# Kernel tuning notes

Hardware: AMD Instinct MI355X
Metric: run time of the kernel (lower is better)

Reference implementation:

```python
import jax, jax.numpy as jnp
import numpy as np

N, F, FE, NB = 50000, 64, 64, 16
E, T = 1_600_000, 1_000_000
IN_DIM = F + 2 * FE + NB  # 208
VAR = 0.15
EPS = 1e-5  # BatchNorm eps


def setup_inputs() -> dict:
    key = jax.random.key(0)
    ks = jax.random.split(key, 10)
    atom_fea = jax.random.normal(ks[0], (N, F), dtype=jnp.float32)
    edge_fea = jax.random.normal(ks[1], (E, FE), dtype=jnp.float32)
    r_ij = jax.random.normal(ks[2], (E, 3), dtype=jnp.float32)
    dist = jax.random.uniform(ks[3], (E,), dtype=jnp.float32, minval=0.5, maxval=5.0)
    cutoff_w = jax.random.uniform(ks[4], (E,), dtype=jnp.float32)
    fc_w = jax.random.normal(ks[5], (2 * F, IN_DIM), dtype=jnp.float32) / np.sqrt(IN_DIM)
    fc_b = jax.random.normal(ks[6], (2 * F,), dtype=jnp.float32) * 0.01
    bn1_gamma = jnp.ones((2 * F,), jnp.float32)
    bn1_beta = jnp.zeros((2 * F,), jnp.float32)
    bn2_gamma = jnp.ones((F,), jnp.float32)
    bn2_beta = jnp.zeros((F,), jnp.float32)
    edge_index = jax.random.randint(ks[7], (2, E), 0, N, dtype=jnp.int32)
    triplet_idx = jax.random.randint(ks[8], (2, T), 0, E, dtype=jnp.int32)
    return dict(atom_fea=atom_fea, edge_fea=edge_fea, r_ij=r_ij, dist=dist,
                cutoff_w=cutoff_w, fc_w=fc_w, fc_b=fc_b,
                bn1_gamma=bn1_gamma, bn1_beta=bn1_beta,
                bn2_gamma=bn2_gamma, bn2_beta=bn2_beta,
                edge_index=edge_index, triplet_idx=triplet_idx)


def _batchnorm(x, gamma, beta):
    # training-mode BatchNorm1d: biased batch statistics
    mu = x.mean(axis=0)
    var = ((x - mu) ** 2).mean(axis=0)
    return (x - mu) * jax.lax.rsqrt(var + EPS) * gamma + beta


def reference(atom_fea, edge_fea, r_ij, dist, cutoff_w, fc_w, fc_b,
              bn1_gamma, bn1_beta, bn2_gamma, bn2_beta,
              edge_index, triplet_idx):
    e1, e2 = triplet_idx[0], triplet_idx[1]
    dst = edge_index[1]
    # angle between neighbour displacement vectors
    v1 = r_ij[e1]            # (T,3)
    v2 = r_ij[e2]            # (T,3)
    d1 = jnp.maximum(dist[e1], 1e-8)
    d2 = jnp.maximum(dist[e2], 1e-8)
    cos_angle = jnp.clip((v1 * v2).sum(-1) / (d1 * d2), -1.0, 1.0)  # (T,)
    centers = jnp.linspace(-1.0, 1.0, NB)
    ang_fea = jnp.exp(-((cos_angle[:, None] - centers) ** 2) / (VAR ** 2))  # (T,NB)
    centre_atoms = dst[e1]   # (T,)
    triplet_fea = jnp.concatenate(
        [atom_fea[centre_atoms], edge_fea[e1], edge_fea[e2], ang_fea], axis=1)  # (T, IN_DIM)
    triplet_fea = _batchnorm(triplet_fea @ fc_w.T + fc_b, bn1_gamma, bn1_beta)  # (T, 2F)
    gate = jax.nn.sigmoid(triplet_fea[:, :F])
    core = jax.nn.softplus(triplet_fea[:, F:])
    messages = gate * core
    messages = messages * (cutoff_w[e1] * cutoff_w[e2])[:, None]
    aggr = jax.ops.segment_sum(messages, centre_atoms, num_segments=N)  # (N,F)
    aggr = _batchnorm(aggr, bn2_gamma, bn2_beta)
    return jax.nn.softplus(atom_fea + aggr)
```

## Files before the change

kernel.cpp:

```cpp
#include <hip/hip_runtime.h>
#include <hip/hip_bf16.h>
#include <math.h>

typedef __bf16 bf16;
typedef __bf16 bf16x8 __attribute__((ext_vector_type(8)));
typedef float  f32x4  __attribute__((ext_vector_type(4)));
typedef float  f32x4e __attribute__((ext_vector_type(4)));

#define MT     64
#define ROWPAD 232
#define NREP   32

union PK8 { bf16 h[8]; uint4 u; };
union PKH { _Float16 h[2]; unsigned int u; };

__device__ inline uint4 pack8(const float4 a, const float4 b) {
  PK8 p;
  p.h[0] = (bf16)a.x; p.h[1] = (bf16)a.y; p.h[2] = (bf16)a.z; p.h[3] = (bf16)a.w;
  p.h[4] = (bf16)b.x; p.h[5] = (bf16)b.y; p.h[6] = (bf16)b.z; p.h[7] = (bf16)b.w;
  return p.u;
}

__device__ inline bf16x8 zero_bf16x8() {
  PK8 z; z.u = make_uint4(0u, 0u, 0u, 0u);
  return *(bf16x8*)z.h;
}

__global__ __launch_bounds__(256)
void k_cvt(const float* __restrict__ src, bf16* __restrict__ dst, long n8) {
  const long i = (long)blockIdx.x * 256 + threadIdx.x;
  if (i >= n8) return;
  const f32x4e a = __builtin_nontemporal_load((const f32x4e*)(src + i * 8));
  const f32x4e b = __builtin_nontemporal_load((const f32x4e*)(src + i * 8 + 4));
  PK8 p;
#pragma unroll
  for (int j = 0; j < 4; ++j) { p.h[j] = (bf16)a[j]; p.h[4 + j] = (bf16)b[j]; }
  *(uint4*)(dst + i * 8) = p.u;
}

__global__ __launch_bounds__(256)
void k_cvtw(const float* __restrict__ fc_w, bf16* __restrict__ dst) {
  const int i = blockIdx.x * 256 + threadIdx.x;
  if (i >= 128 * 28) return;
  const int row = i / 28, c = i - row * 28;
  uint4 v;
  if (c < 26) {
    const float4* p = (const float4*)(fc_w + (size_t)row * 208 + c * 8);
    v = pack8(p[0], p[1]);
  } else {
    v = make_uint4(0u, 0u, 0u, 0u);
  }
  *(uint4*)(dst + (size_t)row * 224 + c * 8) = v;
}

template<bool PRE>
__global__ __launch_bounds__(256)
void k_gemm(const float* __restrict__ atom_fea,
            const float* __restrict__ edge_fea,
            const bf16*  __restrict__ atom_bf,
            const bf16*  __restrict__ edge_bf,
            const float* __restrict__ r_ij,
            const float* __restrict__ dist,
            const float* __restrict__ cutoff_w,
            const float* __restrict__ fc_w,
            const bf16*  __restrict__ fcw_bf,
            const float* __restrict__ fc_b,
            const int*  __restrict__ eidx_dst,
            const int*  __restrict__ trip_e1,
            const int*  __restrict__ trip_e2,
            float* __restrict__ stat1,
            unsigned int* __restrict__ zbuf,
            int*   __restrict__ centre,
            float* __restrict__ cwbuf)
{
  __shared__ __align__(16) bf16 smA[MT * ROWPAD];

  const int tid  = threadIdx.x;
  const int lane = tid & 63;
  const int wv   = tid >> 6;
  const int quad = lane >> 4;
  const int l16  = lane & 15;
  const int t0   = blockIdx.x * MT;

  bf16x8 bfrag[2][7];
  float  bias_v[2];
#pragma unroll
  for (int ns = 0; ns < 2; ++ns) {
    const int col = wv * 32 + ns * 16 + l16;
    bias_v[ns] = fc_b[col];
#pragma unroll
    for (int kc = 0; kc < 7; ++kc) {
      if (PRE) {
        bfrag[ns][kc] = *(const bf16x8*)(fcw_bf + (size_t)col * 224 + kc * 32 + quad * 8);
      } else {
        const int k0 = kc * 32 + quad * 8;
        if (k0 < 208) {
          const float4* p = (const float4*)(fc_w + (size_t)col * 208 + k0);
          PK8 pk; pk.u = pack8(p[0], p[1]);
          bfrag[ns][kc] = *(bf16x8*)pk.h;
        } else {
          bfrag[ns][kc] = zero_bf16x8();
        }
      }
    }
  }

  if (PRE) {
    const int row = tid >> 2;
    const int cq  = tid & 3;
    const int t   = t0 + row;
    const int e1  = trip_e1[t];
    const int e2  = trip_e2[t];
    const int ca  = eidx_dst[e1];
    const bf16* ar = atom_bf + (size_t)ca * 64;
    const bf16* r1 = edge_bf + (size_t)e1 * 64;
    const bf16* r2 = edge_bf + (size_t)e2 * 64;
    const uint4 v0 = *(const uint4*)(ar + cq * 8);
    const uint4 v1 = *(const uint4*)(ar + (cq + 4) * 8);
    const uint4 v2 = *(const uint4*)(r1 + cq * 8);
    const uint4 v3 = *(const uint4*)(r1 + (cq + 4) * 8);
    const uint4 v4 = *(const uint4*)(r2 + cq * 8);
    const uint4 v5 = *(const uint4*)(r2 + (cq + 4) * 8);
    bf16* dstr = smA + row * ROWPAD;
    if (cq == 0) {
      const float x1 = r_ij[e1 * 3], y1 = r_ij[e1 * 3 + 1], z1 = r_ij[e1 * 3 + 2];
      const float x2 = r_ij[e2 * 3], y2 = r_ij[e2 * 3 + 1], z2 = r_ij[e2 * 3 + 2];
      const float d1 = fmaxf(dist[e1], 1e-8f);
      const float d2 = fmaxf(dist[e2], 1e-8f);
      float cv = (x1 * x2 + y1 * y2 + z1 * z2) / (d1 * d2);
      cv = fminf(1.f, fmaxf(-1.f, cv));
      PK8 pa, pb;
#pragma unroll
      for (int j = 0; j < 8; ++j) {
        const float ca0 = cv - (-1.f + (float)j * (2.f / 15.f));
        const float ca1 = cv - (-1.f + (float)(j + 8) * (2.f / 15.f));
        pa.h[j] = (bf16)__expf(-(ca0 * ca0) * 44.4444444f);
        pb.h[j] = (bf16)__expf(-(ca1 * ca1) * 44.4444444f);
      }
      *(uint4*)(dstr + 24 * 8) = pa.u;
      *(uint4*)(dstr + 25 * 8) = pb.u;
      centre[t] = ca;
      cwbuf[t] = cutoff_w[e1] * cutoff_w[e2];
    } else if (cq == 2) {
      *(uint4*)(dstr + 26 * 8) = make_uint4(0u, 0u, 0u, 0u);
    } else if (cq == 3) {
      *(uint4*)(dstr + 27 * 8) = make_uint4(0u, 0u, 0u, 0u);
    }
    *(uint4*)(dstr + cq * 8)        = v0;
    *(uint4*)(dstr + (cq + 4) * 8)  = v1;
    *(uint4*)(dstr + (cq + 8) * 8)  = v2;
    *(uint4*)(dstr + (cq + 12) * 8) = v3;
    *(uint4*)(dstr + (cq + 16) * 8) = v4;
    *(uint4*)(dstr + (cq + 20) * 8) = v5;
  } else {
    for (int i = tid; i < MT * 28; i += 256) {
      const int row = i / 28;
      const int c   = i - row * 28;
      const int t   = t0 + row;
      uint4 val;
      if (c < 8) {
        const int e1 = trip_e1[t];
        const int ca = eidx_dst[e1];
        const float4* p = (const float4*)(atom_fea + (size_t)ca * 64 + c * 8);
        val = pack8(p[0], p[1]);
        if (c == 0) {
          const int e2 = trip_e2[t];
          centre[t] = ca;
          cwbuf[t] = cutoff_w[e1] * cutoff_w[e2];
        }
      } else if (c < 16) {
        const int e1 = trip_e1[t];
        const float4* p = (const float4*)(edge_fea + (size_t)e1 * 64 + (c - 8) * 8);
        val = pack8(p[0], p[1]);
      } else if (c < 24) {
        const int e2 = trip_e2[t];
        const float4* p = (const float4*)(edge_fea + (size_t)e2 * 64 + (c - 16) * 8);
        val = pack8(p[0], p[1]);
      } else if (c < 26) {
        const int e1 = trip_e1[t];
        const int e2 = trip_e2[t];
        const float x1 = r_ij[e1 * 3], y1 = r_ij[e1 * 3 + 1], z1 = r_ij[e1 * 3 + 2];
        const float x2 = r_ij[e2 * 3], y2 = r_ij[e2 * 3 + 1], z2 = r_ij[e2 * 3 + 2];
        const float d1 = fmaxf(dist[e1], 1e-8f);
        const float d2 = fmaxf(dist[e2], 1e-8f);
        float cv = (x1 * x2 + y1 * y2 + z1 * z2) / (d1 * d2);
        cv = fminf(1.f, fmaxf(-1.f, cv));
        PK8 p;
        const int b0 = (c - 24) * 8;
#pragma unroll
        for (int j = 0; j < 8; ++j) {
          const float ctr = -1.f + (float)(b0 + j) * (2.f / 15.f);
          const float dd = cv - ctr;
          p.h[j] = (bf16)__expf(-(dd * dd) * 44.4444444f);
        }
        val = p.u;
      } else {
        val = make_uint4(0u, 0u, 0u, 0u);
      }
      *(uint4*)(smA + row * ROWPAD + c * 8) = val;
    }
  }
  __syncthreads();

  f32x4 acc[4][2] = {};
#pragma unroll
  for (int kc = 0; kc < 7; ++kc) {
    bf16x8 afr[4];
#pragma unroll
    for (int ms = 0; ms < 4; ++ms)
      afr[ms] = *(const bf16x8*)(smA + (ms * 16 + l16) * ROWPAD + kc * 32 + quad * 8);
#pragma unroll
    for (int ms = 0; ms < 4; ++ms)
#pragma unroll
      for (int ns = 0; ns < 2; ++ns)
        acc[ms][ns] = __builtin_amdgcn_mfma_f32_16x16x32_bf16(afr[ms], bfrag[ns][kc], acc[ms][ns], 0, 0, 0);
  }

  unsigned int* zw = zbuf + (size_t)t0 * 64;
  float s0 = 0.f, s20 = 0.f, s1 = 0.f, s21 = 0.f;
#pragma unroll
  for (int ms = 0; ms < 4; ++ms)
#pragma unroll
    for (int r = 0; r < 4; ++r) {
      const float z0 = acc[ms][0][r] + bias_v[0];
      const float z1 = acc[ms][1][r] + bias_v[1];
      PKH pk; pk.h[0] = (_Float16)z0; pk.h[1] = (_Float16)z1;
      const int row = ms * 16 + quad * 4 + r;
      __builtin_nontemporal_store(pk.u, zw + (size_t)row * 64 + wv * 16 + l16);
      s0 += z0; s20 += z0 * z0; s1 += z1; s21 += z1 * z1;
    }
  s0  += __shfl_xor(s0, 16);  s0  += __shfl_xor(s0, 32);
  s20 += __shfl_xor(s20, 16); s20 += __shfl_xor(s20, 32);
  s1  += __shfl_xor(s1, 16);  s1  += __shfl_xor(s1, 32);
  s21 += __shfl_xor(s21, 16); s21 += __shfl_xor(s21, 32);
  if (quad == 0) {
    float* sb = stat1 + (size_t)(blockIdx.x & (NREP - 1)) * 256;
    const int c0 = wv * 32 + l16;
    atomicAdd(sb + c0, s0);
    atomicAdd(sb + 128 + c0, s20);
    atomicAdd(sb + c0 + 16, s1);
    atomicAdd(sb + 128 + c0 + 16, s21);
  }
}

__global__ void k_fin1(const float* __restrict__ stat1,
                       const float* __restrict__ g1, const float* __restrict__ b1,
                       float* __restrict__ bn1sc, float* __restrict__ bn1sh, float invT) {
  const int j = threadIdx.x;
  float s = 0.f, s2 = 0.f;
  for (int r = 0; r < NREP; ++r) { s += stat1[r * 256 + j]; s2 += stat1[r * 256 + 128 + j]; }
  const float mu  = s * invT;
  const float var = fmaxf(s2 * invT - mu * mu, 0.f);
  const float sc  = g1[j] * rsqrtf(var + 1e-5f);
  bn1sc[j] = sc;
  bn1sh[j] = b1[j] - mu * sc;
}

__global__ __launch_bounds__(256)
void k_apply(const unsigned int* __restrict__ zbuf,
             const int*   __restrict__ centre,
             const float* __restrict__ cwbuf,
             const float* __restrict__ bn1sc, const float* __restrict__ bn1sh,
             float* __restrict__ aggr, size_t repN, int T)
{
  const int lane = threadIdx.x & 63;
  const int sub  = threadIdx.x >> 6;
  const int f    = lane;
  const int wg   = ((f >> 5) << 4) | (f & 15);
  const int sel  = (f >> 4) & 1;
  const float scg = bn1sc[f],      shg = bn1sh[f];
  const float scc = bn1sc[64 + f], shc = bn1sh[64 + f];
  float* ag = aggr + (size_t)(blockIdx.x & 1) * repN;
  for (int t = blockIdx.x * 4 + sub; t < T; t += gridDim.x * 4) {
    const unsigned int ug = __builtin_nontemporal_load(zbuf + (size_t)t * 64 + wg);
    const unsigned int uc = __builtin_nontemporal_load(zbuf + (size_t)t * 64 + 32 + wg);
    PKH a, b; a.u = ug; b.u = uc;
    const float zg = (sel ? (float)a.h[1] : (float)a.h[0]) * scg + shg;
    const float zc = (sel ? (float)b.h[1] : (float)b.h[0]) * scc + shc;
    const float gate = 1.f / (1.f + __expf(-zg));
    const float core = (zc > 20.f) ? zc : log1pf(__expf(zc));
    atomicAdd(ag + (size_t)centre[t] * 64 + f, gate * core * cwbuf[t]);
  }
}

__global__ __launch_bounds__(256)
void k_bn2stats(float* __restrict__ aggr, size_t repN, float* __restrict__ stat2, int N) {
  const int col = threadIdx.x & 63;
  const int rg  = threadIdx.x >> 6;
  float s = 0.f, s2 = 0.f;
  for (int n = blockIdx.x * 4 + rg; n < N; n += gridDim.x * 4) {
    const size_t idx = (size_t)n * 64 + col;
    const float v = aggr[idx] + aggr[repN + idx];
    aggr[idx] = v;
    s += v; s2 += v * v;
  }
  __shared__ float ps[4][64], ps2[4][64];
  ps[rg][col] = s; ps2[rg][col] = s2;
  __syncthreads();
  if (rg == 0) {
    s  = ps[0][col] + ps[1][col] + ps[2][col] + ps[3][col];
    s2 = ps2[0][col] + ps2[1][col] + ps2[2][col] + ps2[3][col];
    atomicAdd(stat2 + col, s);
    atomicAdd(stat2 + 64 + col, s2);
  }
}

__global__ __launch_bounds__(256)
void k_final(const float* __restrict__ aggr, const float* __restrict__ atom,
             const float* __restrict__ stat2,
             const float* __restrict__ g2, const float* __restrict__ b2,
             float* __restrict__ out, int total, float invN) {
  const int idx = blockIdx.x * 256 + threadIdx.x;
  if (idx >= total) return;
  const int col = idx & 63;
  const float mu  = stat2[col] * invN;
  const float var = fmaxf(stat2[64 + col] * invN - mu * mu, 0.f);
  const float sc  = g2[col] * rsqrtf(var + 1e-5f);
  const float sh  = b2[col] - mu * sc;
  const float x   = aggr[idx] * sc + sh + atom[idx];
  out[idx] = (x > 20.f) ? x : log1pf(__expf(x));
}

extern "C" void kernel_launch(void* const* d_in, const int* in_sizes, int n_in,
                              void* d_out, int out_size, void* d_ws, size_t ws_size,
                              hipStream_t stream) {
  const float* atom_fea = (const float*)d_in[0];
  const float* edge_fea = (const float*)d_in[1];
  const float* r_ij     = (const float*)d_in[2];
  const float* dist     = (const float*)d_in[3];
  const float* cutoff_w = (const float*)d_in[4];
  const float* fc_w     = (const float*)d_in[5];
  const float* fc_b     = (const float*)d_in[6];
  const float* bn1g     = (const float*)d_in[7];
  const float* bn1b     = (const float*)d_in[8];
  const float* bn2g     = (const float*)d_in[9];
  const float* bn2b     = (const float*)d_in[10];
  const int*  eidx      = (const int*)d_in[11];
  const int*  tidx      = (const int*)d_in[12];

  const int N = in_sizes[0] / 64;
  const int E = in_sizes[3];
  const int T = in_sizes[12] / 2;

  const size_t repN = (size_t)N * 64;

  size_t off = 0;
  char* base = (char*)d_ws;
  auto carve = [&](size_t bytes) -> void* {
    void* p = base + off;
    off += (bytes + 255) & ~(size_t)255;
    return p;
  };
  float* aggr    = (float*)carve(2 * repN * 4);
  float* stat1   = (float*)carve((size_t)NREP * 256 * 4);
  float* bn1sc   = (float*)carve(128 * 4);
  float* bn1sh   = (float*)carve(128 * 4);
  float* stat2   = (float*)carve(128 * 4);
  float* cwbuf   = (float*)carve((size_t)T * 4);
  int*   centre  = (int*)carve((size_t)T * 4);
  unsigned int* zbuf = (unsigned int*)carve((size_t)T * 64 * 4);
  bf16*  edge_bf = (bf16*)carve((size_t)E * 64 * 2);
  bf16*  atom_bf = (bf16*)carve((size_t)N * 64 * 2);
  bf16*  fcw_bf  = (bf16*)carve((size_t)128 * 224 * 2);
  const bool pre = (off <= ws_size);

  hipMemsetAsync(aggr,  0, 2 * repN * sizeof(float), stream);
  hipMemsetAsync(stat1, 0, (size_t)NREP * 256 * sizeof(float), stream);
  hipMemsetAsync(stat2, 0, 128 * sizeof(float), stream);

  const int nblk = T / MT;
  if (pre) {
    const long e8 = (long)E * 64 / 8;
    const long a8 = (long)N * 64 / 8;
    k_cvt<<<(int)((e8 + 255) / 256), 256, 0, stream>>>(edge_fea, edge_bf, e8);
    k_cvt<<<(int)((a8 + 255) / 256), 256, 0, stream>>>(atom_fea, atom_bf, a8);
    k_cvtw<<<14, 256, 0, stream>>>(fc_w, fcw_bf);
    k_gemm<true><<<nblk, 256, 0, stream>>>(atom_fea, edge_fea, atom_bf, edge_bf,
                                           r_ij, dist, cutoff_w, fc_w, fcw_bf, fc_b,
                                           eidx + E, tidx, tidx + T,
                                           stat1, zbuf, centre, cwbuf);
  } else {
    k_gemm<false><<<nblk, 256, 0, stream>>>(atom_fea, edge_fea, atom_bf, edge_bf,
                                            r_ij, dist, cutoff_w, fc_w, fcw_bf, fc_b,
                                            eidx + E, tidx, tidx + T,
                                            stat1, zbuf, centre, cwbuf);
  }
  k_fin1<<<1, 128, 0, stream>>>(stat1, bn1g, bn1b, bn1sc, bn1sh, 1.0f / (float)T);
  k_apply<<<4096, 256, 0, stream>>>(zbuf, centre, cwbuf, bn1sc, bn1sh, aggr, repN, T);
  k_bn2stats<<<256, 256, 0, stream>>>(aggr, repN, stat2, N);
  const int total = N * 64;
  k_final<<<(total + 255) / 256, 256, 0, stream>>>(aggr, atom_fea, stat2, bn2g, bn2b,
                                                   (float*)d_out, total, 1.0f / (float)N);
}
```

Measured before the change: 1.099 ms.

## Replace atomic segment-sum with counting-sort CSR segmented reduction

```diff
diff --git a/kernel.cpp b/kernel.cpp
--- a/kernel.cpp
+++ b/kernel.cpp
@@ -24,6 +24,13 @@
 __device__ inline bf16x8 zero_bf16x8() {
   PK8 z; z.u = make_uint4(0u, 0u, 0u, 0u);
   return *(bf16x8*)z.h;
+}
+
+__device__ inline float fsigmoid(float x) {
+  return __builtin_amdgcn_rcpf(1.f + __expf(-x));
+}
+__device__ inline float fsoftplus(float x) {
+  return (x > 20.f) ? x : __logf(1.f + __expf(x));
 }
 
 __global__ __launch_bounds__(256)
@@ -53,6 +60,67 @@
   *(uint4*)(dst + (size_t)row * 224 + c * 8) = v;
 }
 
+__global__ __launch_bounds__(256)
+void k_prep(const int* __restrict__ trip_e1, const int* __restrict__ trip_e2,
+            const int* __restrict__ eidx_dst, const float* __restrict__ cutoff_w,
+            int* __restrict__ centre, float* __restrict__ cwbuf,
+            int* __restrict__ cnt, int T) {
+  for (int t = blockIdx.x * 256 + threadIdx.x; t < T; t += gridDim.x * 256) {
+    const int e1 = trip_e1[t];
+    const int e2 = trip_e2[t];
+    const int ca = eidx_dst[e1];
+    centre[t] = ca;
+    cwbuf[t] = cutoff_w[e1] * cutoff_w[e2];
+    atomicAdd(cnt + ca, 1);
+  }
+}
+
+__global__ __launch_bounds__(1024)
+void k_scan(const int* __restrict__ cnt, int* __restrict__ off,
+            int* __restrict__ cnt2, int N) {
+  __shared__ int part[1024];
+  const int tid = threadIdx.x;
+  const int CH  = (N + 1023) >> 10;
+  const int base = tid * CH;
+  int s = 0;
+  for (int i = 0; i < CH; ++i) {
+    const int idx = base + i;
+    if (idx < N) s += cnt[idx];
+  }
+  part[tid] = s;
+  __syncthreads();
+  for (int d = 1; d < 1024; d <<= 1) {
+    const int v = part[tid];
+    const int w = (tid >= d) ? part[tid - d] : 0;
+    __syncthreads();
+    part[tid] = v + w;
+    __syncthreads();
+  }
+  int run = (tid == 0) ? 0 : part[tid - 1];
+  for (int i = 0; i < CH; ++i) {
+    const int idx = base + i;
+    if (idx < N) {
+      const int c = cnt[idx];
+      off[idx] = run;
+      cnt2[idx] = run;
+      run += c;
+    }
+  }
+  if (tid == 1023) off[N] = run;
+}
+
+__global__ __launch_bounds__(256)
+void k_scatter(const int* __restrict__ centre, const float* __restrict__ cwbuf,
+               int* __restrict__ cnt2, int* __restrict__ post,
+               float* __restrict__ cw_s, int T) {
+  for (int t = blockIdx.x * 256 + threadIdx.x; t < T; t += gridDim.x * 256) {
+    const int c = centre[t];
+    const int p = atomicAdd(cnt2 + c, 1);
+    post[t] = p;
+    cw_s[p] = cwbuf[t];
+  }
+}
+
 template<bool PRE>
 __global__ __launch_bounds__(256)
 void k_gemm(const float* __restrict__ atom_fea,
@@ -61,19 +129,18 @@
             const bf16*  __restrict__ edge_bf,
             const float* __restrict__ r_ij,
             const float* __restrict__ dist,
-            const float* __restrict__ cutoff_w,
             const float* __restrict__ fc_w,
             const bf16*  __restrict__ fcw_bf,
             const float* __restrict__ fc_b,
-            const int*  __restrict__ eidx_dst,
             const int*  __restrict__ trip_e1,
             const int*  __restrict__ trip_e2,
+            const int*  __restrict__ centre,
+            const int*  __restrict__ post,
             float* __restrict__ stat1,
-            unsigned int* __restrict__ zbuf,
-            int*   __restrict__ centre,
-            float* __restrict__ cwbuf)
+            unsigned int* __restrict__ zbuf)
 {
   __shared__ __align__(16) bf16 smA[MT * ROWPAD];
+  __shared__ int sPos[MT];
 
   const int tid  = threadIdx.x;
   const int lane = tid & 63;
@@ -111,7 +178,7 @@
     const int t   = t0 + row;
     const int e1  = trip_e1[t];
     const int e2  = trip_e2[t];
-    const int ca  = eidx_dst[e1];
+    const int ca  = centre[t];
     const bf16* ar = atom_bf + (size_t)ca * 64;
     const bf16* r1 = edge_bf + (size_t)e1 * 64;
     const bf16* r2 = edge_bf + (size_t)e2 * 64;
@@ -139,8 +206,7 @@
       }
       *(uint4*)(dstr + 24 * 8) = pa.u;
       *(uint4*)(dstr + 25 * 8) = pb.u;
-      centre[t] = ca;
-      cwbuf[t] = cutoff_w[e1] * cutoff_w[e2];
+      sPos[row] = post[t];
     } else if (cq == 2) {
       *(uint4*)(dstr + 26 * 8) = make_uint4(0u, 0u, 0u, 0u);
     } else if (cq == 3) {
@@ -159,15 +225,10 @@
       const int t   = t0 + row;
       uint4 val;
       if (c < 8) {
-        const int e1 = trip_e1[t];
-        const int ca = eidx_dst[e1];
+        const int ca = centre[t];
         const float4* p = (const float4*)(atom_fea + (size_t)ca * 64 + c * 8);
         val = pack8(p[0], p[1]);
-        if (c == 0) {
-          const int e2 = trip_e2[t];
-          centre[t] = ca;
-          cwbuf[t] = cutoff_w[e1] * cutoff_w[e2];
-        }
+        if (c == 0) sPos[row] = post[t];
       } else if (c < 16) {
         const int e1 = trip_e1[t];
         const float4* p = (const float4*)(edge_fea + (size_t)e1 * 64 + (c - 8) * 8);
@@ -216,7 +277,6 @@
         acc[ms][ns] = __builtin_amdgcn_mfma_f32_16x16x32_bf16(afr[ms], bfrag[ns][kc], acc[ms][ns], 0, 0, 0);
   }
 
-  unsigned int* zw = zbuf + (size_t)t0 * 64;
   float s0 = 0.f, s20 = 0.f, s1 = 0.f, s21 = 0.f;
 #pragma unroll
   for (int ms = 0; ms < 4; ++ms)
@@ -226,7 +286,7 @@
       const float z1 = acc[ms][1][r] + bias_v[1];
       PKH pk; pk.h[0] = (_Float16)z0; pk.h[1] = (_Float16)z1;
       const int row = ms * 16 + quad * 4 + r;
-      __builtin_nontemporal_store(pk.u, zw + (size_t)row * 64 + wv * 16 + l16);
+      __builtin_nontemporal_store(pk.u, zbuf + (size_t)sPos[row] * 64 + wv * 16 + l16);
       s0 += z0; s20 += z0 * z0; s1 += z1; s21 += z1 * z1;
     }
   s0  += __shfl_xor(s0, 16);  s0  += __shfl_xor(s0, 32);
@@ -257,41 +317,39 @@
 }
 
 __global__ __launch_bounds__(256)
-void k_apply(const unsigned int* __restrict__ zbuf,
-             const int*   __restrict__ centre,
-             const float* __restrict__ cwbuf,
-             const float* __restrict__ bn1sc, const float* __restrict__ bn1sh,
-             float* __restrict__ aggr, size_t repN, int T)
+void k_apply2(const unsigned int* __restrict__ zbuf,
+              const int*   __restrict__ off,
+              const float* __restrict__ cw_s,
+              const float* __restrict__ bn1sc, const float* __restrict__ bn1sh,
+              float* __restrict__ aggr, int N)
 {
-  const int lane = threadIdx.x & 63;
-  const int sub  = threadIdx.x >> 6;
-  const int f    = lane;
-  const int wg   = ((f >> 5) << 4) | (f & 15);
-  const int sel  = (f >> 4) & 1;
+  const int n = (blockIdx.x << 2) | (threadIdx.x >> 6);
+  if (n >= N) return;
+  const int f   = threadIdx.x & 63;
+  const int wg  = ((f >> 5) << 4) | (f & 15);
+  const int sel = (f >> 4) & 1;
   const float scg = bn1sc[f],      shg = bn1sh[f];
   const float scc = bn1sc[64 + f], shc = bn1sh[64 + f];
-  float* ag = aggr + (size_t)(blockIdx.x & 1) * repN;
-  for (int t = blockIdx.x * 4 + sub; t < T; t += gridDim.x * 4) {
-    const unsigned int ug = __builtin_nontemporal_load(zbuf + (size_t)t * 64 + wg);
-    const unsigned int uc = __builtin_nontemporal_load(zbuf + (size_t)t * 64 + 32 + wg);
+  const int i0 = off[n], i1 = off[n + 1];
+  float acc = 0.f;
+  for (int i = i0; i < i1; ++i) {
+    const unsigned int ug = __builtin_nontemporal_load(zbuf + (size_t)i * 64 + wg);
+    const unsigned int uc = __builtin_nontemporal_load(zbuf + (size_t)i * 64 + 32 + wg);
     PKH a, b; a.u = ug; b.u = uc;
     const float zg = (sel ? (float)a.h[1] : (float)a.h[0]) * scg + shg;
     const float zc = (sel ? (float)b.h[1] : (float)b.h[0]) * scc + shc;
-    const float gate = 1.f / (1.f + __expf(-zg));
-    const float core = (zc > 20.f) ? zc : log1pf(__expf(zc));
-    atomicAdd(ag + (size_t)centre[t] * 64 + f, gate * core * cwbuf[t]);
-  }
-}
-
-__global__ __launch_bounds__(256)
-void k_bn2stats(float* __restrict__ aggr, size_t repN, float* __restrict__ stat2, int N) {
+    acc += fsigmoid(zg) * fsoftplus(zc) * cw_s[i];
+  }
+  aggr[(size_t)n * 64 + f] = acc;
+}
+
+__global__ __launch_bounds__(256)
+void k_bn2stats(const float* __restrict__ aggr, float* __restrict__ stat2, int N) {
   const int col = threadIdx.x & 63;
   const int rg  = threadIdx.x >> 6;
   float s = 0.f, s2 = 0.f;
   for (int n = blockIdx.x * 4 + rg; n < N; n += gridDim.x * 4) {
-    const size_t idx = (size_t)n * 64 + col;
-    const float v = aggr[idx] + aggr[repN + idx];
-    aggr[idx] = v;
+    const float v = aggr[(size_t)n * 64 + col];
     s += v; s2 += v * v;
   }
   __shared__ float ps[4][64], ps2[4][64];
@@ -318,7 +376,7 @@
   const float sc  = g2[col] * rsqrtf(var + 1e-5f);
   const float sh  = b2[col] - mu * sc;
   const float x   = aggr[idx] * sc + sh + atom[idx];
-  out[idx] = (x > 20.f) ? x : log1pf(__expf(x));
+  out[idx] = fsoftplus(x);
 }
 
 extern "C" void kernel_launch(void* const* d_in, const int* in_sizes, int n_in,
@@ -342,29 +400,32 @@
   const int E = in_sizes[3];
   const int T = in_sizes[12] / 2;
 
-  const size_t repN = (size_t)N * 64;
-
-  size_t off = 0;
+  size_t off_b = 0;
   char* base = (char*)d_ws;
   auto carve = [&](size_t bytes) -> void* {
-    void* p = base + off;
-    off += (bytes + 255) & ~(size_t)255;
+    void* p = base + off_b;
+    off_b += (bytes + 255) & ~(size_t)255;
     return p;
   };
-  float* aggr    = (float*)carve(2 * repN * 4);
+  float* aggr    = (float*)carve((size_t)N * 64 * 4);
   float* stat1   = (float*)carve((size_t)NREP * 256 * 4);
   float* bn1sc   = (float*)carve(128 * 4);
   float* bn1sh   = (float*)carve(128 * 4);
   float* stat2   = (float*)carve(128 * 4);
+  int*   cnt     = (int*)carve((size_t)N * 4);
+  int*   offs    = (int*)carve((size_t)(N + 1) * 4);
+  int*   cnt2    = (int*)carve((size_t)N * 4);
+  int*   centre  = (int*)carve((size_t)T * 4);
   float* cwbuf   = (float*)carve((size_t)T * 4);
-  int*   centre  = (int*)carve((size_t)T * 4);
+  int*   post    = (int*)carve((size_t)T * 4);
+  float* cw_s    = (float*)carve((size_t)T * 4);
   unsigned int* zbuf = (unsigned int*)carve((size_t)T * 64 * 4);
   bf16*  edge_bf = (bf16*)carve((size_t)E * 64 * 2);
   bf16*  atom_bf = (bf16*)carve((size_t)N * 64 * 2);
   bf16*  fcw_bf  = (bf16*)carve((size_t)128 * 224 * 2);
-  const bool pre = (off <= ws_size);
-
-  hipMemsetAsync(aggr,  0, 2 * repN * sizeof(float), stream);
+  const bool pre = (off_b <= ws_size);
+
+  hipMemsetAsync(cnt,   0, (size_t)N * 4, stream);
   hipMemsetAsync(stat1, 0, (size_t)NREP * 256 * sizeof(float), stream);
   hipMemsetAsync(stat2, 0, 128 * sizeof(float), stream);
 
@@ -375,19 +436,25 @@
     k_cvt<<<(int)((e8 + 255) / 256), 256, 0, stream>>>(edge_fea, edge_bf, e8);
     k_cvt<<<(int)((a8 + 255) / 256), 256, 0, stream>>>(atom_fea, atom_bf, a8);
     k_cvtw<<<14, 256, 0, stream>>>(fc_w, fcw_bf);
+  }
+  k_prep<<<2048, 256, 0, stream>>>(tidx, tidx + T, eidx + E, cutoff_w,
+                                   centre, cwbuf, cnt, T);
+  k_scan<<<1, 1024, 0, stream>>>(cnt, offs, cnt2, N);
+  k_scatter<<<2048, 256, 0, stream>>>(centre, cwbuf, cnt2, post, cw_s, T);
+  if (pre) {
     k_gemm<true><<<nblk, 256, 0, stream>>>(atom_fea, edge_fea, atom_bf, edge_bf,
-                                           r_ij, dist, cutoff_w, fc_w, fcw_bf, fc_b,
-                                           eidx + E, tidx, tidx + T,
-                                           stat1, zbuf, centre, cwbuf);
+                                           r_ij, dist, fc_w, fcw_bf, fc_b,
+                                           tidx, tidx + T, centre, post,
+                                           stat1, zbuf);
   } else {
     k_gemm<false><<<nblk, 256, 0, stream>>>(atom_fea, edge_fea, atom_bf, edge_bf,
-                                            r_ij, dist, cutoff_w, fc_w, fcw_bf, fc_b,
-                                            eidx + E, tidx, tidx + T,
-                                            stat1, zbuf, centre, cwbuf);
+                                            r_ij, dist, fc_w, fcw_bf, fc_b,
+                                            tidx, tidx + T, centre, post,
+                                            stat1, zbuf);
   }
   k_fin1<<<1, 128, 0, stream>>>(stat1, bn1g, bn1b, bn1sc, bn1sh, 1.0f / (float)T);
-  k_apply<<<4096, 256, 0, stream>>>(zbuf, centre, cwbuf, bn1sc, bn1sh, aggr, repN, T);
-  k_bn2stats<<<256, 256, 0, stream>>>(aggr, repN, stat2, N);
+  k_apply2<<<(N + 3) / 4, 256, 0, stream>>>(zbuf, offs, cw_s, bn1sc, bn1sh, aggr, N);
+  k_bn2stats<<<256, 256, 0, stream>>>(aggr, stat2, N);
   const int total = N * 64;
   k_final<<<(total + 255) / 256, 256, 0, stream>>>(aggr, atom_fea, stat2, bn2g, bn2b,
                                                    (float*)d_out, total, 1.0f / (float)N);
```

After: 1.170 ms. 1.06x slower.
